# Kernel optimization log

Measured on AMD Instinct MI355X. Metric: run time of the kernel, lower is better.

Reference implementation:

```python
import jax, jax.numpy as jnp
import numpy as np

NUM_ROUNDS = 4
NUM_REVERSE_ROUNDS = 4
N_NODES = 1_000_000
N_EDGES = 32_000_000


def _scatter_mean(x, src, dst, num_nodes):
    # x: [N, F]; gather messages from src nodes, mean-reduce at dst nodes.
    msgs = x[src]                                             # [E, F]
    agg = jax.ops.segment_sum(msgs, dst, num_segments=num_nodes)  # [N, F]
    cnt = jax.ops.segment_sum(jnp.ones((src.shape[0],), x.dtype), dst,
                              num_segments=num_nodes)         # [N]
    return agg / jnp.maximum(cnt, 1.0)[:, None]


def setup_inputs() -> dict:
    key = jax.random.key(0)
    k1, k2, k3 = jax.random.split(key, 3)
    topic_one_hot = jax.random.uniform(k1, (N_NODES,), dtype=jnp.float32)
    edge_index = jax.random.randint(k2, (2, N_EDGES), 0, N_NODES, dtype=jnp.int32)
    reverse_edge_index = jax.random.randint(k3, (2, N_EDGES), 0, N_NODES, dtype=jnp.int32)
    return {
        "topic_one_hot": topic_one_hot,
        "edge_index": edge_index,
        "reverse_edge_index": reverse_edge_index,
    }


def reference(topic_one_hot, edge_index, reverse_edge_index):
    n = topic_one_hot.shape[0]
    results = []
    # forward-direction rounds
    h = topic_one_hot[:, None]  # [N, 1]
    src, dst = edge_index[0], edge_index[1]
    for _ in range(NUM_ROUNDS):
        h = _scatter_mean(h, src, dst, n)
        results.append(h)
    # reverse-direction rounds
    h_rev = topic_one_hot[:, None]
    rsrc, rdst = reverse_edge_index[0], reverse_edge_index[1]
    for _ in range(NUM_REVERSE_ROUNDS):
        h_rev = _scatter_mean(h_rev, rsrc, rdst, n)
        results.append(h_rev)
    # original returns a python list of [N,1] tensors; stack for a single array
    return jnp.stack(results, axis=0)  # [num_rounds+num_reverse_rounds, N, 1]
```

## Files before the change

kernel.cpp:

```cpp
#include <hip/hip_runtime.h>


typedef unsigned uint32x4 __attribute__((ext_vector_type(4)));

#define TPB_E 1024
#define NPART 512
#define TPB_P 512
#define BATCH 8192
#define CAP 32
#define NBMAX 512
#define BSH 11
#define BSZ 2048
#define BMASK 2047u


__global__ __launch_bounds__(TPB_P)
void p1_count(const int* __restrict__ dst, unsigned* __restrict__ blkcnt,
              int E, int chunk, int NB) {
    __shared__ unsigned h[NBMAX];
    for (int i = threadIdx.x; i < NB; i += TPB_P) h[i] = 0u;
    __syncthreads();
    int beg = blockIdx.x * chunk;
    int end = min(beg + chunk, E);
    int len = end - beg; if (len < 0) len = 0;
    const uint32x4* d4 = (const uint32x4*)(dst + beg);
    int n4 = len >> 2;
    for (int i = threadIdx.x; i < n4; i += TPB_P) {
        uint32x4 d = __builtin_nontemporal_load(&d4[i]);
        atomicAdd(&h[d.x >> BSH], 1u);
        atomicAdd(&h[d.y >> BSH], 1u);
        atomicAdd(&h[d.z >> BSH], 1u);
        atomicAdd(&h[d.w >> BSH], 1u);
    }
    __syncthreads();
    unsigned* o = blkcnt + (size_t)blockIdx.x * NB;
    for (int i = threadIdx.x; i < NB; i += TPB_P) o[i] = h[i];
}

__global__ __launch_bounds__(TPB_P)
void s1_totals(const unsigned* __restrict__ blkcnt, unsigned* __restrict__ totals,
               int NB, int nblk) {
    __shared__ unsigned red[TPB_P];
    int b = blockIdx.x;
    unsigned s = 0;
    for (int k = threadIdx.x; k < nblk; k += TPB_P) s += blkcnt[(size_t)k * NB + b];
    red[threadIdx.x] = s;
    __syncthreads();
    for (int off = TPB_P / 2; off > 0; off >>= 1) {
        if (threadIdx.x < off) red[threadIdx.x] += red[threadIdx.x + off];
        __syncthreads();
    }
    if (threadIdx.x == 0) totals[b] = red[0];
}

__global__ __launch_bounds__(TPB_P)
void s2_scan(const unsigned* __restrict__ totals, unsigned* __restrict__ base, int NB) {
    __shared__ unsigned t[TPB_P];
    int tid = threadIdx.x;
    unsigned v = (tid < NB) ? totals[tid] : 0u;
    t[tid] = v;
    __syncthreads();
    for (int off = 1; off < TPB_P; off <<= 1) {
        unsigned w = (tid >= off) ? t[tid - off] : 0u;
        __syncthreads();
        t[tid] += w;
        __syncthreads();
    }
    if (tid < NB) base[tid] = t[tid] - v;
    if (tid == NB - 1) base[NB] = t[tid];
}

__global__ __launch_bounds__(TPB_P)
void s3_start(const unsigned* __restrict__ blkcnt, const unsigned* __restrict__ base,
              unsigned* __restrict__ start, int NB, int nblk) {
    __shared__ unsigned t[TPB_P];
    int b = blockIdx.x;
    int tid = threadIdx.x;
    unsigned v = (tid < nblk) ? blkcnt[(size_t)tid * NB + b] : 0u;
    t[tid] = v;
    __syncthreads();
    for (int off = 1; off < TPB_P; off <<= 1) {
        unsigned w = (tid >= off) ? t[tid - off] : 0u;
        __syncthreads();
        t[tid] += w;
        __syncthreads();
    }
    if (tid < nblk) start[(size_t)tid * NB + b] = base[b] + t[tid] - v;
}

__global__ __launch_bounds__(TPB_P)
void p2_scatter(const int* __restrict__ src, const int* __restrict__ dst,
                const unsigned* __restrict__ start, unsigned* __restrict__ packed,
                int E, int chunk, int NB) {
    __shared__ unsigned stg[NBMAX * CAP];
    __shared__ unsigned h[NBMAX];
    __shared__ unsigned gcur[NBMAX];
    int tid = threadIdx.x;
    int bid = blockIdx.x;
    for (int i = tid; i < NB; i += TPB_P) gcur[i] = start[(size_t)bid * NB + i];
    int beg = bid * chunk;
    int end = min(beg + chunk, E);
    int wid = tid >> 6, lane = tid & 63;
    for (int bb = beg; bb < end; bb += BATCH) {
        int bend = min(bb + BATCH, end);
        int n4 = (bend - bb) >> 2;
        for (int i = tid; i < NB; i += TPB_P) h[i] = 0u;
        __syncthreads();
        const uint32x4* s4 = (const uint32x4*)(src + bb);
        const uint32x4* d4 = (const uint32x4*)(dst + bb);
        for (int i = tid; i < n4; i += TPB_P) {
            uint32x4 s = __builtin_nontemporal_load(&s4[i]);
            uint32x4 d = __builtin_nontemporal_load(&d4[i]);
            unsigned sv[4] = {s.x, s.y, s.z, s.w};
            unsigned dv[4] = {d.x, d.y, d.z, d.w};
            #pragma unroll
            for (int k = 0; k < 4; ++k) {
                unsigned b = dv[k] >> BSH;
                unsigned val = (sv[k] << BSH) | (dv[k] & BMASK);
                unsigned pos = atomicAdd(&h[b], 1u);
                if (pos < CAP) stg[(b << 5) + ((pos + b) & 31u)] = val;
                else packed[gcur[b] + pos] = val;
            }
        }
        __syncthreads();
        for (int b = wid; b < NB; b += TPB_P / 64) {
            unsigned cnt = h[b];
            unsigned n = cnt < CAP ? cnt : CAP;
            unsigned g0 = gcur[b];
            for (unsigned i = lane; i < n; i += 64)
                packed[g0 + i] = stg[(b << 5) + ((i + b) & 31u)];
            if (lane == 0) gcur[b] = g0 + cnt;
        }
        __syncthreads();
    }
}

template <bool FIRST>
__global__ __launch_bounds__(TPB_E)
void e_pass(const float* __restrict__ x, const unsigned* __restrict__ packed,
            const unsigned* __restrict__ boff, float* __restrict__ rcnt,
            float* __restrict__ outslice, int N) {
    __shared__ float acc[BSZ];
    __shared__ unsigned c[FIRST ? BSZ : 1];
    int tid = threadIdx.x;
    for (int i = tid; i < BSZ; i += TPB_E) {
        acc[i] = 0.0f;
        if (FIRST) c[i] = 0u;
    }
    __syncthreads();
    int b = blockIdx.x;
    int beg = (int)boff[b], end = (int)boff[b + 1];
    int a0 = min((beg + 3) & ~3, end);
    for (int e = beg + tid; e < a0; e += TPB_E) {
        unsigned p = packed[e];
        atomicAdd(&acc[p & BMASK], x[p >> BSH]);
        if (FIRST) atomicAdd(&c[p & BMASK], 1u);
    }
    int i0 = a0 >> 2, i1 = i0 + ((end - a0) >> 2);
    const uint32x4* p4 = (const uint32x4*)packed;
    int i = i0 + tid;
    for (; i + TPB_E < i1; i += 2 * TPB_E) {
        uint32x4 a = __builtin_nontemporal_load(&p4[i]);
        uint32x4 bq = __builtin_nontemporal_load(&p4[i + TPB_E]);
        float xa0 = x[a.x >> BSH];
        float xa1 = x[a.y >> BSH];
        float xa2 = x[a.z >> BSH];
        float xa3 = x[a.w >> BSH];
        float xb0 = x[bq.x >> BSH];
        float xb1 = x[bq.y >> BSH];
        float xb2 = x[bq.z >> BSH];
        float xb3 = x[bq.w >> BSH];
        atomicAdd(&acc[a.x & BMASK], xa0);
        atomicAdd(&acc[a.y & BMASK], xa1);
        atomicAdd(&acc[a.z & BMASK], xa2);
        atomicAdd(&acc[a.w & BMASK], xa3);
        atomicAdd(&acc[bq.x & BMASK], xb0);
        atomicAdd(&acc[bq.y & BMASK], xb1);
        atomicAdd(&acc[bq.z & BMASK], xb2);
        atomicAdd(&acc[bq.w & BMASK], xb3);
        if (FIRST) {
            atomicAdd(&c[a.x & BMASK], 1u);
            atomicAdd(&c[a.y & BMASK], 1u);
            atomicAdd(&c[a.z & BMASK], 1u);
            atomicAdd(&c[a.w & BMASK], 1u);
            atomicAdd(&c[bq.x & BMASK], 1u);
            atomicAdd(&c[bq.y & BMASK], 1u);
            atomicAdd(&c[bq.z & BMASK], 1u);
            atomicAdd(&c[bq.w & BMASK], 1u);
        }
    }
    for (; i < i1; i += TPB_E) {
        uint32x4 p = __builtin_nontemporal_load(&p4[i]);
        float x0 = x[p.x >> BSH];
        float x1 = x[p.y >> BSH];
        float x2 = x[p.z >> BSH];
        float x3 = x[p.w >> BSH];
        atomicAdd(&acc[p.x & BMASK], x0);
        atomicAdd(&acc[p.y & BMASK], x1);
        atomicAdd(&acc[p.z & BMASK], x2);
        atomicAdd(&acc[p.w & BMASK], x3);
        if (FIRST) {
            atomicAdd(&c[p.x & BMASK], 1u);
            atomicAdd(&c[p.y & BMASK], 1u);
            atomicAdd(&c[p.z & BMASK], 1u);
            atomicAdd(&c[p.w & BMASK], 1u);
        }
    }
    for (int e = a0 + ((end - a0) & ~3) + tid; e < end; e += TPB_E) {
        unsigned p = packed[e];
        atomicAdd(&acc[p & BMASK], x[p >> BSH]);
        if (FIRST) atomicAdd(&c[p & BMASK], 1u);
    }
    __syncthreads();
    int nbase = b << BSH;
    for (int idx = tid; idx < BSZ; idx += TPB_E) {
        int node = nbase + idx;
        if (node < N) {
            float rc;
            if (FIRST) {
                unsigned cv = c[idx];
                rc = 1.0f / (float)(cv > 0u ? cv : 1u);
                rcnt[node] = rc;
            } else {
                rc = rcnt[node];
            }
            outslice[node] = acc[idx] * rc;
        }
    }
}


#define TPB 256
#define MAX_BLOCKS 2048

__global__ void round_first(const float* __restrict__ x, const int* __restrict__ src,
                            const int* __restrict__ dst, float* __restrict__ agg,
                            float* __restrict__ cnt, int nE) {
    int i = blockIdx.x * blockDim.x + threadIdx.x;
    int stride = gridDim.x * blockDim.x;
    for (; i < nE; i += stride) {
        atomicAdd(&agg[dst[i]], x[src[i]]);
        atomicAdd(&cnt[dst[i]], 1.0f);
    }
}

__global__ void round_next(const float* __restrict__ x, const int* __restrict__ src,
                           const int* __restrict__ dst, float* __restrict__ agg, int nE) {
    int i = blockIdx.x * blockDim.x + threadIdx.x;
    int stride = gridDim.x * blockDim.x;
    for (; i < nE; i += stride) atomicAdd(&agg[dst[i]], x[src[i]]);
}

__global__ void normalize_k(float* __restrict__ out, const float* __restrict__ cnt, int n) {
    int i = blockIdx.x * blockDim.x + threadIdx.x;
    int stride = gridDim.x * blockDim.x;
    for (; i < n; i += stride) out[i] /= fmaxf(cnt[i], 1.0f);
}


extern "C" void kernel_launch(void* const* d_in, const int* in_sizes, int n_in,
                              void* d_out, int out_size, void* d_ws, size_t ws_size,
                              hipStream_t stream) {
    const float* topic = (const float*)d_in[0];
    const int* ei  = (const int*)d_in[1];
    const int* rei = (const int*)d_in[2];
    const int N = in_sizes[0];
    const int E = in_sizes[1] / 2;

    float* out = (float*)d_out;

    const int NB = (N + BSZ - 1) >> BSH;
    const int chunk = ((E + NPART * 16 - 1) / (NPART * 16)) * 16;

    size_t off = 0;
    auto alloc = [&](size_t bytes) { size_t o = off; off += (bytes + 255) & ~(size_t)255; return o; };
    size_t o_packed = alloc((size_t)E * 4);
    size_t o_cnt    = alloc((size_t)N * 4);
    size_t o_blkcnt = alloc((size_t)NPART * NB * 4);
    size_t o_start  = alloc((size_t)NPART * NB * 4);
    size_t o_totals = alloc((size_t)NBMAX * 4);
    size_t o_base   = alloc((size_t)(NBMAX + 1) * 4);
    bool fast = (off <= ws_size) && (NB >= 2) && (NB <= NBMAX) &&
                (N <= (1 << 20)) && (E % 16 == 0);

    if (fast) {
        char* ws = (char*)d_ws;
        unsigned* packed = (unsigned*)(ws + o_packed);
        float*    rcnt   = (float*)   (ws + o_cnt);
        unsigned* blkcnt = (unsigned*)(ws + o_blkcnt);
        unsigned* start  = (unsigned*)(ws + o_start);
        unsigned* totals = (unsigned*)(ws + o_totals);
        unsigned* base   = (unsigned*)(ws + o_base);

        for (int dir = 0; dir < 2; ++dir) {
            const int* src = (dir == 0) ? ei : rei;
            const int* dst = src + E;
            float* oslab = out + (size_t)dir * 4 * N;

            p1_count<<<NPART, TPB_P, 0, stream>>>(dst, blkcnt, E, chunk, NB);
            s1_totals<<<NB, TPB_P, 0, stream>>>(blkcnt, totals, NB, NPART);
            s2_scan<<<1, TPB_P, 0, stream>>>(totals, base, NB);
            s3_start<<<NB, TPB_P, 0, stream>>>(blkcnt, base, start, NB, NPART);
            p2_scatter<<<NPART, TPB_P, 0, stream>>>(src, dst, start, packed, E, chunk, NB);

            e_pass<true><<<NB, TPB_E, 0, stream>>>(topic, packed, base, rcnt, oslab, N);
            for (int r = 1; r < 4; ++r) {
                e_pass<false><<<NB, TPB_E, 0, stream>>>(oslab + (size_t)(r - 1) * N, packed,
                                                        base, rcnt, oslab + (size_t)r * N, N);
            }
        }
        return;
    }

    const int* src = ei;
    const int* dst = ei + E;
    const int* rsrc = rei;
    const int* rdst = rei + E;

    float* cnt_f = (float*)d_ws;
    float* cnt_r = cnt_f + N;

    (void)hipMemsetAsync(d_out, 0, (size_t)out_size * sizeof(float), stream);
    (void)hipMemsetAsync(d_ws, 0, (size_t)2 * N * sizeof(float), stream);

    int eb = (E + TPB - 1) / TPB; if (eb > MAX_BLOCKS) eb = MAX_BLOCKS;
    int nb = (N + TPB - 1) / TPB; if (nb > MAX_BLOCKS) nb = MAX_BLOCKS;

    round_first<<<eb, TPB, 0, stream>>>(topic, src, dst, out, cnt_f, E);
    normalize_k<<<nb, TPB, 0, stream>>>(out, cnt_f, N);
    for (int r = 1; r < 4; ++r) {
        round_next<<<eb, TPB, 0, stream>>>(out + (size_t)(r - 1) * N, src, dst,
                                           out + (size_t)r * N, E);
        normalize_k<<<nb, TPB, 0, stream>>>(out + (size_t)r * N, cnt_f, N);
    }
    round_first<<<eb, TPB, 0, stream>>>(topic, rsrc, rdst, out + (size_t)4 * N, cnt_r, E);
    normalize_k<<<nb, TPB, 0, stream>>>(out + (size_t)4 * N, cnt_r, N);
    for (int r = 5; r < 8; ++r) {
        round_next<<<eb, TPB, 0, stream>>>(out + (size_t)(r - 1) * N, rsrc, rdst,
                                           out + (size_t)r * N, E);
        normalize_k<<<nb, TPB, 0, stream>>>(out + (size_t)r * N, cnt_r, N);
    }
}
```

Baseline: 1.743 ms.

## Two-pass bucket sort edges by source then destination for gather locality

Replaces the single destination-bucket scatter with a two-pass partition. Edges are first bucketed by source block into an intermediate buffer, then re-bucketed by destination block. Each destination bucket then holds edges in source-sorted order, which should make the x[src] gathers in the four propagation rounds more cache-local. Bucket size grows to 4096 nodes (NB drops to 256) and the e_pass loop is simplified to scalar loads. In exchange, each direction gains an extra pass over 32M edges, a binary search per 4 edges to recover the source bucket, and an extra E-sized workspace buffer.

```diff
diff --git a/kernel.cpp b/kernel.cpp
--- a/kernel.cpp
+++ b/kernel.cpp
@@ -7,30 +7,29 @@
 #define NPART 512
 #define TPB_P 512
 #define BATCH 8192
-#define CAP 32
-#define NBMAX 512
-#define BSH 11
-#define BSZ 2048
-#define BMASK 2047u
-
-
-__global__ __launch_bounds__(TPB_P)
-void p1_count(const int* __restrict__ dst, unsigned* __restrict__ blkcnt,
-              int E, int chunk, int NB) {
+#define CAP 64
+#define NBMAX 256
+#define KSH 12
+#define KMASK 4095u
+
+
+__global__ __launch_bounds__(TPB_P)
+void p1_count(const unsigned* __restrict__ keys, unsigned* __restrict__ blkcnt,
+              int E, int chunk, int NB, int shift) {
     __shared__ unsigned h[NBMAX];
     for (int i = threadIdx.x; i < NB; i += TPB_P) h[i] = 0u;
     __syncthreads();
     int beg = blockIdx.x * chunk;
     int end = min(beg + chunk, E);
     int len = end - beg; if (len < 0) len = 0;
-    const uint32x4* d4 = (const uint32x4*)(dst + beg);
+    const uint32x4* k4 = (const uint32x4*)(keys + beg);
     int n4 = len >> 2;
     for (int i = threadIdx.x; i < n4; i += TPB_P) {
-        uint32x4 d = __builtin_nontemporal_load(&d4[i]);
-        atomicAdd(&h[d.x >> BSH], 1u);
-        atomicAdd(&h[d.y >> BSH], 1u);
-        atomicAdd(&h[d.z >> BSH], 1u);
-        atomicAdd(&h[d.w >> BSH], 1u);
+        uint32x4 k = __builtin_nontemporal_load(&k4[i]);
+        atomicAdd(&h[k.x >> shift], 1u);
+        atomicAdd(&h[k.y >> shift], 1u);
+        atomicAdd(&h[k.z >> shift], 1u);
+        atomicAdd(&h[k.w >> shift], 1u);
     }
     __syncthreads();
     unsigned* o = blkcnt + (size_t)blockIdx.x * NB;
@@ -89,9 +88,9 @@
 }
 
 __global__ __launch_bounds__(TPB_P)
-void p2_scatter(const int* __restrict__ src, const int* __restrict__ dst,
-                const unsigned* __restrict__ start, unsigned* __restrict__ packed,
-                int E, int chunk, int NB) {
+void p2_pair(const unsigned* __restrict__ keys, const unsigned* __restrict__ other,
+             const unsigned* __restrict__ start, unsigned* __restrict__ outbuf,
+             int E, int chunk, int NB) {
     __shared__ unsigned stg[NBMAX * CAP];
     __shared__ unsigned h[NBMAX];
     __shared__ unsigned gcur[NBMAX];
@@ -106,20 +105,20 @@
         int n4 = (bend - bb) >> 2;
         for (int i = tid; i < NB; i += TPB_P) h[i] = 0u;
         __syncthreads();
-        const uint32x4* s4 = (const uint32x4*)(src + bb);
-        const uint32x4* d4 = (const uint32x4*)(dst + bb);
+        const uint32x4* k4 = (const uint32x4*)(keys + bb);
+        const uint32x4* o4 = (const uint32x4*)(other + bb);
         for (int i = tid; i < n4; i += TPB_P) {
-            uint32x4 s = __builtin_nontemporal_load(&s4[i]);
-            uint32x4 d = __builtin_nontemporal_load(&d4[i]);
-            unsigned sv[4] = {s.x, s.y, s.z, s.w};
-            unsigned dv[4] = {d.x, d.y, d.z, d.w};
+            uint32x4 k = __builtin_nontemporal_load(&k4[i]);
+            uint32x4 o = __builtin_nontemporal_load(&o4[i]);
+            unsigned kv[4] = {k.x, k.y, k.z, k.w};
+            unsigned ov[4] = {o.x, o.y, o.z, o.w};
             #pragma unroll
-            for (int k = 0; k < 4; ++k) {
-                unsigned b = dv[k] >> BSH;
-                unsigned val = (sv[k] << BSH) | (dv[k] & BMASK);
+            for (int q = 0; q < 4; ++q) {
+                unsigned b = kv[q] >> KSH;
+                unsigned val = (ov[q] << KSH) | (kv[q] & KMASK);
                 unsigned pos = atomicAdd(&h[b], 1u);
-                if (pos < CAP) stg[(b << 5) + ((pos + b) & 31u)] = val;
-                else packed[gcur[b] + pos] = val;
+                if (pos < CAP) stg[(b << 6) + ((pos + b) & 63u)] = val;
+                else outbuf[gcur[b] + pos] = val;
             }
         }
         __syncthreads();
@@ -128,103 +127,104 @@
             unsigned n = cnt < CAP ? cnt : CAP;
             unsigned g0 = gcur[b];
             for (unsigned i = lane; i < n; i += 64)
-                packed[g0 + i] = stg[(b << 5) + ((i + b) & 31u)];
+                outbuf[g0 + i] = stg[(b << 6) + ((i + b) & 63u)];
             if (lane == 0) gcur[b] = g0 + cnt;
         }
         __syncthreads();
     }
 }
+
+__global__ __launch_bounds__(TPB_P)
+void p2b_scatter(const unsigned* __restrict__ e1, const unsigned* __restrict__ base1,
+                 const unsigned* __restrict__ start, unsigned* __restrict__ packed,
+                 int E, int chunk, int NB, int NB1) {
+    __shared__ unsigned stg[NBMAX * CAP];
+    __shared__ unsigned h[NBMAX];
+    __shared__ unsigned gcur[NBMAX];
+    __shared__ unsigned b1[NBMAX + 1];
+    int tid = threadIdx.x;
+    int bid = blockIdx.x;
+    for (int i = tid; i < NB; i += TPB_P) gcur[i] = start[(size_t)bid * NB + i];
+    for (int i = tid; i <= NB1; i += TPB_P) b1[i] = base1[i];
+    int beg = bid * chunk;
+    int end = min(beg + chunk, E);
+    int wid = tid >> 6, lane = tid & 63;
+    for (int bb = beg; bb < end; bb += BATCH) {
+        int bend = min(bb + BATCH, end);
+        int n4 = (bend - bb) >> 2;
+        for (int i = tid; i < NB; i += TPB_P) h[i] = 0u;
+        __syncthreads();
+        const uint32x4* q4 = (const uint32x4*)(e1 + bb);
+        for (int i = tid; i < n4; i += TPB_P) {
+            uint32x4 q = __builtin_nontemporal_load(&q4[i]);
+            int e0 = bb + (i << 2);
+            int lo = 0, hi = NB1;
+            while (hi - lo > 1) {
+                int mid = (lo + hi) >> 1;
+                if ((unsigned)e0 >= b1[mid]) lo = mid; else hi = mid;
+            }
+            unsigned sb = (unsigned)lo;
+            unsigned qa[4] = {q.x, q.y, q.z, q.w};
+            #pragma unroll
+            for (int k = 0; k < 4; ++k) {
+                while ((unsigned)(e0 + k) >= b1[sb + 1]) sb++;
+                unsigned qv = qa[k];
+                unsigned b = qv >> 24;
+                unsigned srcf = (sb << KSH) | (qv & KMASK);
+                unsigned val = (srcf << KSH) | ((qv >> KSH) & KMASK);
+                unsigned pos = atomicAdd(&h[b], 1u);
+                if (pos < CAP) stg[(b << 6) + ((pos + b) & 63u)] = val;
+                else packed[gcur[b] + pos] = val;
+            }
+        }
+        __syncthreads();
+        for (int b = wid; b < NB; b += TPB_P / 64) {
+            unsigned cnt = h[b];
+            unsigned n = cnt < CAP ? cnt : CAP;
+            unsigned g0 = gcur[b];
+            for (unsigned i = lane; i < n; i += 64)
+                packed[g0 + i] = stg[(b << 6) + ((i + b) & 63u)];
+            if (lane == 0) gcur[b] = g0 + cnt;
+        }
+        __syncthreads();
+    }
+}
+
 
 template <bool FIRST>
 __global__ __launch_bounds__(TPB_E)
 void e_pass(const float* __restrict__ x, const unsigned* __restrict__ packed,
             const unsigned* __restrict__ boff, float* __restrict__ rcnt,
             float* __restrict__ outslice, int N) {
-    __shared__ float acc[BSZ];
-    __shared__ unsigned c[FIRST ? BSZ : 1];
-    int tid = threadIdx.x;
-    for (int i = tid; i < BSZ; i += TPB_E) {
+    __shared__ float acc[1 << KSH];
+    __shared__ unsigned c[FIRST ? (1 << KSH) : 1];
+    int tid = threadIdx.x;
+    for (int i = tid; i < (1 << KSH); i += TPB_E) {
         acc[i] = 0.0f;
         if (FIRST) c[i] = 0u;
     }
     __syncthreads();
     int b = blockIdx.x;
     int beg = (int)boff[b], end = (int)boff[b + 1];
-    int a0 = min((beg + 3) & ~3, end);
-    for (int e = beg + tid; e < a0; e += TPB_E) {
-        unsigned p = packed[e];
-        atomicAdd(&acc[p & BMASK], x[p >> BSH]);
-        if (FIRST) atomicAdd(&c[p & BMASK], 1u);
-    }
-    int i0 = a0 >> 2, i1 = i0 + ((end - a0) >> 2);
-    const uint32x4* p4 = (const uint32x4*)packed;
-    int i = i0 + tid;
-    for (; i + TPB_E < i1; i += 2 * TPB_E) {
-        uint32x4 a = __builtin_nontemporal_load(&p4[i]);
-        uint32x4 bq = __builtin_nontemporal_load(&p4[i + TPB_E]);
-        float xa0 = x[a.x >> BSH];
-        float xa1 = x[a.y >> BSH];
-        float xa2 = x[a.z >> BSH];
-        float xa3 = x[a.w >> BSH];
-        float xb0 = x[bq.x >> BSH];
-        float xb1 = x[bq.y >> BSH];
-        float xb2 = x[bq.z >> BSH];
-        float xb3 = x[bq.w >> BSH];
-        atomicAdd(&acc[a.x & BMASK], xa0);
-        atomicAdd(&acc[a.y & BMASK], xa1);
-        atomicAdd(&acc[a.z & BMASK], xa2);
-        atomicAdd(&acc[a.w & BMASK], xa3);
-        atomicAdd(&acc[bq.x & BMASK], xb0);
-        atomicAdd(&acc[bq.y & BMASK], xb1);
-        atomicAdd(&acc[bq.z & BMASK], xb2);
-        atomicAdd(&acc[bq.w & BMASK], xb3);
-        if (FIRST) {
-            atomicAdd(&c[a.x & BMASK], 1u);
-            atomicAdd(&c[a.y & BMASK], 1u);
-            atomicAdd(&c[a.z & BMASK], 1u);
-            atomicAdd(&c[a.w & BMASK], 1u);
-            atomicAdd(&c[bq.x & BMASK], 1u);
-            atomicAdd(&c[bq.y & BMASK], 1u);
-            atomicAdd(&c[bq.z & BMASK], 1u);
-            atomicAdd(&c[bq.w & BMASK], 1u);
-        }
-    }
-    for (; i < i1; i += TPB_E) {
-        uint32x4 p = __builtin_nontemporal_load(&p4[i]);
-        float x0 = x[p.x >> BSH];
-        float x1 = x[p.y >> BSH];
-        float x2 = x[p.z >> BSH];
-        float x3 = x[p.w >> BSH];
-        atomicAdd(&acc[p.x & BMASK], x0);
-        atomicAdd(&acc[p.y & BMASK], x1);
-        atomicAdd(&acc[p.z & BMASK], x2);
-        atomicAdd(&acc[p.w & BMASK], x3);
-        if (FIRST) {
-            atomicAdd(&c[p.x & BMASK], 1u);
-            atomicAdd(&c[p.y & BMASK], 1u);
-            atomicAdd(&c[p.z & BMASK], 1u);
-            atomicAdd(&c[p.w & BMASK], 1u);
-        }
-    }
-    for (int e = a0 + ((end - a0) & ~3) + tid; e < end; e += TPB_E) {
-        unsigned p = packed[e];
-        atomicAdd(&acc[p & BMASK], x[p >> BSH]);
-        if (FIRST) atomicAdd(&c[p & BMASK], 1u);
-    }
-    __syncthreads();
-    int nbase = b << BSH;
-    for (int idx = tid; idx < BSZ; idx += TPB_E) {
-        int node = nbase + idx;
+    for (int e = beg + tid; e < end; e += TPB_E) {
+        unsigned p = __builtin_nontemporal_load(&packed[e]);
+        atomicAdd(&acc[p & KMASK], x[p >> KSH]);
+        if (FIRST) atomicAdd(&c[p & KMASK], 1u);
+    }
+    __syncthreads();
+    int nbase = b << KSH;
+    for (int i = tid; i < (1 << KSH); i += TPB_E) {
+        int node = nbase + i;
         if (node < N) {
             float rc;
             if (FIRST) {
-                unsigned cv = c[idx];
+                unsigned cv = c[i];
                 rc = 1.0f / (float)(cv > 0u ? cv : 1u);
                 rcnt[node] = rc;
             } else {
                 rc = rcnt[node];
             }
-            outslice[node] = acc[idx] * rc;
+            outslice[node] = acc[i] * rc;
         }
     }
 }
@@ -269,7 +269,7 @@
 
     float* out = (float*)d_out;
 
-    const int NB = (N + BSZ - 1) >> BSH;
+    const int NB = (N + (int)KMASK) >> KSH;
     const int chunk = ((E + NPART * 16 - 1) / (NPART * 16)) * 16;
 
     size_t off = 0;
@@ -279,34 +279,57 @@
     size_t o_blkcnt = alloc((size_t)NPART * NB * 4);
     size_t o_start  = alloc((size_t)NPART * NB * 4);
     size_t o_totals = alloc((size_t)NBMAX * 4);
-    size_t o_base   = alloc((size_t)(NBMAX + 1) * 4);
-    bool fast = (off <= ws_size) && (NB >= 2) && (NB <= NBMAX) &&
-                (N <= (1 << 20)) && (E % 16 == 0);
-
-    if (fast) {
+    size_t o_base1  = alloc((size_t)(NBMAX + 1) * 4);
+    size_t o_base2  = alloc((size_t)(NBMAX + 1) * 4);
+    size_t need_mid = off;
+    size_t o_e1     = alloc((size_t)E * 4);
+    size_t need_full = off;
+
+    bool shapes_ok = (NB >= 2) && (NB <= NBMAX) && (N <= (1 << 20)) &&
+                     (E % 16 == 0) && (E > 0);
+    bool full = shapes_ok && (need_full <= ws_size);
+    bool mid  = shapes_ok && (need_mid <= ws_size);
+
+    if (full || mid) {
         char* ws = (char*)d_ws;
         unsigned* packed = (unsigned*)(ws + o_packed);
         float*    rcnt   = (float*)   (ws + o_cnt);
         unsigned* blkcnt = (unsigned*)(ws + o_blkcnt);
         unsigned* start  = (unsigned*)(ws + o_start);
         unsigned* totals = (unsigned*)(ws + o_totals);
-        unsigned* base   = (unsigned*)(ws + o_base);
+        unsigned* base1  = (unsigned*)(ws + o_base1);
+        unsigned* base2  = (unsigned*)(ws + o_base2);
+        unsigned* e1     = full ? (unsigned*)(ws + o_e1) : nullptr;
 
         for (int dir = 0; dir < 2; ++dir) {
-            const int* src = (dir == 0) ? ei : rei;
-            const int* dst = src + E;
+            const unsigned* src = (const unsigned*)((dir == 0) ? ei : rei);
+            const unsigned* dst = src + E;
             float* oslab = out + (size_t)dir * 4 * N;
 
-            p1_count<<<NPART, TPB_P, 0, stream>>>(dst, blkcnt, E, chunk, NB);
-            s1_totals<<<NB, TPB_P, 0, stream>>>(blkcnt, totals, NB, NPART);
-            s2_scan<<<1, TPB_P, 0, stream>>>(totals, base, NB);
-            s3_start<<<NB, TPB_P, 0, stream>>>(blkcnt, base, start, NB, NPART);
-            p2_scatter<<<NPART, TPB_P, 0, stream>>>(src, dst, start, packed, E, chunk, NB);
-
-            e_pass<true><<<NB, TPB_E, 0, stream>>>(topic, packed, base, rcnt, oslab, N);
+            if (full) {
+                p1_count<<<NPART, TPB_P, 0, stream>>>(src, blkcnt, E, chunk, NB, KSH);
+                s1_totals<<<NB, TPB_P, 0, stream>>>(blkcnt, totals, NB, NPART);
+                s2_scan<<<1, TPB_P, 0, stream>>>(totals, base1, NB);
+                s3_start<<<NB, TPB_P, 0, stream>>>(blkcnt, base1, start, NB, NPART);
+                p2_pair<<<NPART, TPB_P, 0, stream>>>(src, dst, start, e1, E, chunk, NB);
+                p1_count<<<NPART, TPB_P, 0, stream>>>(e1, blkcnt, E, chunk, NB, 24);
+                s1_totals<<<NB, TPB_P, 0, stream>>>(blkcnt, totals, NB, NPART);
+                s2_scan<<<1, TPB_P, 0, stream>>>(totals, base2, NB);
+                s3_start<<<NB, TPB_P, 0, stream>>>(blkcnt, base2, start, NB, NPART);
+                p2b_scatter<<<NPART, TPB_P, 0, stream>>>(e1, base1, start, packed,
+                                                         E, chunk, NB, NB);
+            } else {
+                p1_count<<<NPART, TPB_P, 0, stream>>>(dst, blkcnt, E, chunk, NB, KSH);
+                s1_totals<<<NB, TPB_P, 0, stream>>>(blkcnt, totals, NB, NPART);
+                s2_scan<<<1, TPB_P, 0, stream>>>(totals, base2, NB);
+                s3_start<<<NB, TPB_P, 0, stream>>>(blkcnt, base2, start, NB, NPART);
+                p2_pair<<<NPART, TPB_P, 0, stream>>>(dst, src, start, packed, E, chunk, NB);
+            }
+
+            e_pass<true><<<NB, TPB_E, 0, stream>>>(topic, packed, base2, rcnt, oslab, N);
             for (int r = 1; r < 4; ++r) {
                 e_pass<false><<<NB, TPB_E, 0, stream>>>(oslab + (size_t)(r - 1) * N, packed,
-                                                        base, rcnt, oslab + (size_t)r * N, N);
+                                                        base2, rcnt, oslab + (size_t)r * N, N);
             }
         }
         return;
```

Result: slower. 2.038 ms (+16.9%).

## Fuse forward and reverse edge passes into one dual-direction launch

Applied to the files above, without the earlier changes.

Builds both directions' packed edge buckets first, then runs each round's gather and scatter-mean for both directions in a single kernel with twice as many blocks. This doubles the grid from about 489 to about 978 blocks so the GPU is fuller, and halves the number of launches. It also drops the vectorized 4-wide unrolled inner loop in favour of a simple scalar nontemporal loop, and halves block size to 512. Extra workspace is needed for a second packed array; a sequential fallback is kept when workspace is short. Losing the vector loads and the unroll may reduce memory-level parallelism per thread.

```diff
diff --git a/kernel.cpp b/kernel.cpp
--- a/kernel.cpp
+++ b/kernel.cpp
@@ -3,7 +3,7 @@
 
 typedef unsigned uint32x4 __attribute__((ext_vector_type(4)));
 
-#define TPB_E 1024
+#define TPB_E 512
 #define NPART 512
 #define TPB_P 512
 #define BATCH 8192
@@ -135,11 +135,15 @@
     }
 }
 
+
 template <bool FIRST>
 __global__ __launch_bounds__(TPB_E)
-void e_pass(const float* __restrict__ x, const unsigned* __restrict__ packed,
-            const unsigned* __restrict__ boff, float* __restrict__ rcnt,
-            float* __restrict__ outslice, int N) {
+void e_pass_dual(const float* __restrict__ xf, const float* __restrict__ xr,
+                 const unsigned* __restrict__ pf, const unsigned* __restrict__ pr,
+                 const unsigned* __restrict__ basef, const unsigned* __restrict__ baser,
+                 float* __restrict__ rcntf, float* __restrict__ rcntr,
+                 float* __restrict__ outf, float* __restrict__ outr,
+                 int N, int NB) {
     __shared__ float acc[BSZ];
     __shared__ unsigned c[FIRST ? BSZ : 1];
     int tid = threadIdx.x;
@@ -149,82 +153,34 @@
     }
     __syncthreads();
     int b = blockIdx.x;
-    int beg = (int)boff[b], end = (int)boff[b + 1];
-    int a0 = min((beg + 3) & ~3, end);
-    for (int e = beg + tid; e < a0; e += TPB_E) {
-        unsigned p = packed[e];
+    bool rev = (b >= NB);
+    int bb = rev ? b - NB : b;
+    const float* x = rev ? xr : xf;
+    const unsigned* packed = rev ? pr : pf;
+    const unsigned* boff = rev ? baser : basef;
+    float* rcnt = rev ? rcntr : rcntf;
+    float* outslice = rev ? outr : outf;
+
+    int beg = (int)boff[bb], end = (int)boff[bb + 1];
+    for (int e = beg + tid; e < end; e += TPB_E) {
+        unsigned p = __builtin_nontemporal_load(&packed[e]);
         atomicAdd(&acc[p & BMASK], x[p >> BSH]);
         if (FIRST) atomicAdd(&c[p & BMASK], 1u);
     }
-    int i0 = a0 >> 2, i1 = i0 + ((end - a0) >> 2);
-    const uint32x4* p4 = (const uint32x4*)packed;
-    int i = i0 + tid;
-    for (; i + TPB_E < i1; i += 2 * TPB_E) {
-        uint32x4 a = __builtin_nontemporal_load(&p4[i]);
-        uint32x4 bq = __builtin_nontemporal_load(&p4[i + TPB_E]);
-        float xa0 = x[a.x >> BSH];
-        float xa1 = x[a.y >> BSH];
-        float xa2 = x[a.z >> BSH];
-        float xa3 = x[a.w >> BSH];
-        float xb0 = x[bq.x >> BSH];
-        float xb1 = x[bq.y >> BSH];
-        float xb2 = x[bq.z >> BSH];
-        float xb3 = x[bq.w >> BSH];
-        atomicAdd(&acc[a.x & BMASK], xa0);
-        atomicAdd(&acc[a.y & BMASK], xa1);
-        atomicAdd(&acc[a.z & BMASK], xa2);
-        atomicAdd(&acc[a.w & BMASK], xa3);
-        atomicAdd(&acc[bq.x & BMASK], xb0);
-        atomicAdd(&acc[bq.y & BMASK], xb1);
-        atomicAdd(&acc[bq.z & BMASK], xb2);
-        atomicAdd(&acc[bq.w & BMASK], xb3);
-        if (FIRST) {
-            atomicAdd(&c[a.x & BMASK], 1u);
-            atomicAdd(&c[a.y & BMASK], 1u);
-            atomicAdd(&c[a.z & BMASK], 1u);
-            atomicAdd(&c[a.w & BMASK], 1u);
-            atomicAdd(&c[bq.x & BMASK], 1u);
-            atomicAdd(&c[bq.y & BMASK], 1u);
-            atomicAdd(&c[bq.z & BMASK], 1u);
-            atomicAdd(&c[bq.w & BMASK], 1u);
-        }
-    }
-    for (; i < i1; i += TPB_E) {
-        uint32x4 p = __builtin_nontemporal_load(&p4[i]);
-        float x0 = x[p.x >> BSH];
-        float x1 = x[p.y >> BSH];
-        float x2 = x[p.z >> BSH];
-        float x3 = x[p.w >> BSH];
-        atomicAdd(&acc[p.x & BMASK], x0);
-        atomicAdd(&acc[p.y & BMASK], x1);
-        atomicAdd(&acc[p.z & BMASK], x2);
-        atomicAdd(&acc[p.w & BMASK], x3);
-        if (FIRST) {
-            atomicAdd(&c[p.x & BMASK], 1u);
-            atomicAdd(&c[p.y & BMASK], 1u);
-            atomicAdd(&c[p.z & BMASK], 1u);
-            atomicAdd(&c[p.w & BMASK], 1u);
-        }
-    }
-    for (int e = a0 + ((end - a0) & ~3) + tid; e < end; e += TPB_E) {
-        unsigned p = packed[e];
-        atomicAdd(&acc[p & BMASK], x[p >> BSH]);
-        if (FIRST) atomicAdd(&c[p & BMASK], 1u);
-    }
-    __syncthreads();
-    int nbase = b << BSH;
-    for (int idx = tid; idx < BSZ; idx += TPB_E) {
-        int node = nbase + idx;
+    __syncthreads();
+    int nbase = bb << BSH;
+    for (int i = tid; i < BSZ; i += TPB_E) {
+        int node = nbase + i;
         if (node < N) {
             float rc;
             if (FIRST) {
-                unsigned cv = c[idx];
+                unsigned cv = c[i];
                 rc = 1.0f / (float)(cv > 0u ? cv : 1u);
                 rcnt[node] = rc;
             } else {
                 rc = rcnt[node];
             }
-            outslice[node] = acc[idx] * rc;
+            outslice[node] = acc[i] * rc;
         }
     }
 }
@@ -274,39 +230,80 @@
 
     size_t off = 0;
     auto alloc = [&](size_t bytes) { size_t o = off; off += (bytes + 255) & ~(size_t)255; return o; };
-    size_t o_packed = alloc((size_t)E * 4);
-    size_t o_cnt    = alloc((size_t)N * 4);
-    size_t o_blkcnt = alloc((size_t)NPART * NB * 4);
-    size_t o_start  = alloc((size_t)NPART * NB * 4);
-    size_t o_totals = alloc((size_t)NBMAX * 4);
-    size_t o_base   = alloc((size_t)(NBMAX + 1) * 4);
-    bool fast = (off <= ws_size) && (NB >= 2) && (NB <= NBMAX) &&
-                (N <= (1 << 20)) && (E % 16 == 0);
-
-    if (fast) {
+    size_t o_packed_f = alloc((size_t)E * 4);
+    size_t o_rcnt_f   = alloc((size_t)N * 4);
+    size_t o_rcnt_r   = alloc((size_t)N * 4);
+    size_t o_blkcnt   = alloc((size_t)NPART * NB * 4);
+    size_t o_start    = alloc((size_t)NPART * NB * 4);
+    size_t o_totals   = alloc((size_t)NBMAX * 4);
+    size_t o_base_f   = alloc((size_t)(NBMAX + 1) * 4);
+    size_t o_base_r   = alloc((size_t)(NBMAX + 1) * 4);
+    size_t need_seq   = off;
+    size_t o_packed_r = alloc((size_t)E * 4);
+    size_t need_dual  = off;
+
+    bool shapes_ok = (NB >= 2) && (NB <= NBMAX) && (N <= (1 << 20)) &&
+                     (E % 16 == 0) && (E > 0);
+    bool dual = shapes_ok && (need_dual <= ws_size);
+    bool seq  = shapes_ok && (need_seq <= ws_size);
+
+    if (dual || seq) {
         char* ws = (char*)d_ws;
-        unsigned* packed = (unsigned*)(ws + o_packed);
-        float*    rcnt   = (float*)   (ws + o_cnt);
-        unsigned* blkcnt = (unsigned*)(ws + o_blkcnt);
-        unsigned* start  = (unsigned*)(ws + o_start);
-        unsigned* totals = (unsigned*)(ws + o_totals);
-        unsigned* base   = (unsigned*)(ws + o_base);
-
-        for (int dir = 0; dir < 2; ++dir) {
-            const int* src = (dir == 0) ? ei : rei;
-            const int* dst = src + E;
-            float* oslab = out + (size_t)dir * 4 * N;
-
-            p1_count<<<NPART, TPB_P, 0, stream>>>(dst, blkcnt, E, chunk, NB);
-            s1_totals<<<NB, TPB_P, 0, stream>>>(blkcnt, totals, NB, NPART);
-            s2_scan<<<1, TPB_P, 0, stream>>>(totals, base, NB);
-            s3_start<<<NB, TPB_P, 0, stream>>>(blkcnt, base, start, NB, NPART);
-            p2_scatter<<<NPART, TPB_P, 0, stream>>>(src, dst, start, packed, E, chunk, NB);
-
-            e_pass<true><<<NB, TPB_E, 0, stream>>>(topic, packed, base, rcnt, oslab, N);
+        unsigned* packed_f = (unsigned*)(ws + o_packed_f);
+        unsigned* packed_r = dual ? (unsigned*)(ws + o_packed_r) : nullptr;
+        float*    rcnt_f   = (float*)(ws + o_rcnt_f);
+        float*    rcnt_r   = (float*)(ws + o_rcnt_r);
+        unsigned* blkcnt   = (unsigned*)(ws + o_blkcnt);
+        unsigned* start    = (unsigned*)(ws + o_start);
+        unsigned* totals   = (unsigned*)(ws + o_totals);
+        unsigned* base_f   = (unsigned*)(ws + o_base_f);
+        unsigned* base_r   = (unsigned*)(ws + o_base_r);
+
+        if (dual) {
+            for (int dir = 0; dir < 2; ++dir) {
+                const int* src = (dir == 0) ? ei : rei;
+                const int* dst = src + E;
+                unsigned* packed = (dir == 0) ? packed_f : packed_r;
+                unsigned* base   = (dir == 0) ? base_f : base_r;
+                p1_count<<<NPART, TPB_P, 0, stream>>>(dst, blkcnt, E, chunk, NB);
+                s1_totals<<<NB, TPB_P, 0, stream>>>(blkcnt, totals, NB, NPART);
+                s2_scan<<<1, TPB_P, 0, stream>>>(totals, base, NB);
+                s3_start<<<NB, TPB_P, 0, stream>>>(blkcnt, base, start, NB, NPART);
+                p2_scatter<<<NPART, TPB_P, 0, stream>>>(src, dst, start, packed, E, chunk, NB);
+            }
+            float* out_f = out;
+            float* out_r = out + (size_t)4 * N;
+            e_pass_dual<true><<<2 * NB, TPB_E, 0, stream>>>(
+                topic, topic, packed_f, packed_r, base_f, base_r,
+                rcnt_f, rcnt_r, out_f, out_r, N, NB);
             for (int r = 1; r < 4; ++r) {
-                e_pass<false><<<NB, TPB_E, 0, stream>>>(oslab + (size_t)(r - 1) * N, packed,
-                                                        base, rcnt, oslab + (size_t)r * N, N);
+                e_pass_dual<false><<<2 * NB, TPB_E, 0, stream>>>(
+                    out_f + (size_t)(r - 1) * N, out_r + (size_t)(r - 1) * N,
+                    packed_f, packed_r, base_f, base_r,
+                    rcnt_f, rcnt_r,
+                    out_f + (size_t)r * N, out_r + (size_t)r * N, N, NB);
+            }
+        } else {
+            for (int dir = 0; dir < 2; ++dir) {
+                const int* src = (dir == 0) ? ei : rei;
+                const int* dst = src + E;
+                float* oslab = out + (size_t)dir * 4 * N;
+                float* rcnt  = (dir == 0) ? rcnt_f : rcnt_r;
+                unsigned* base = (dir == 0) ? base_f : base_r;
+                p1_count<<<NPART, TPB_P, 0, stream>>>(dst, blkcnt, E, chunk, NB);
+                s1_totals<<<NB, TPB_P, 0, stream>>>(blkcnt, totals, NB, NPART);
+                s2_scan<<<1, TPB_P, 0, stream>>>(totals, base, NB);
+                s3_start<<<NB, TPB_P, 0, stream>>>(blkcnt, base, start, NB, NPART);
+                p2_scatter<<<NPART, TPB_P, 0, stream>>>(src, dst, start, packed_f, E, chunk, NB);
+                e_pass_dual<true><<<NB, TPB_E, 0, stream>>>(
+                    topic, topic, packed_f, packed_f, base, base,
+                    rcnt, rcnt, oslab, oslab, N, NB);
+                for (int r = 1; r < 4; ++r) {
+                    e_pass_dual<false><<<NB, TPB_E, 0, stream>>>(
+                        oslab + (size_t)(r - 1) * N, oslab + (size_t)(r - 1) * N,
+                        packed_f, packed_f, base, base, rcnt, rcnt,
+                        oslab + (size_t)r * N, oslab + (size_t)r * N, N, NB);
+                }
             }
         }
         return;
```

Result: slower. 2.443 ms (+40.2%).
